# Performance work log

Measured on AMD Instinct MI355X. Metric: run time of the kernel, lower is better.

The kernel has to match this reference:

```python
import jax, jax.numpy as jnp
import numpy as np

SUB_NO = 20
T_NO = 200
T_DATA = 200000
E_NO = 400
I_NO = 100
N_BASIS = 20
COS_SHIFT = 1.0
COS_SCALE = 5.0


def make_cos_basis():
    # (N_BASIS, T_NO) raised-cosine basis in log time
    i = jnp.arange(N_BASIS, dtype=jnp.float32)[:, None]
    phi = (jnp.pi / 2.0) * i
    x = jnp.arange(T_NO, dtype=jnp.float32)[None, :]
    raw = COS_SCALE * jnp.log(x + COS_SHIFT)
    basis = 0.5 * jnp.cos(raw - phi) + 0.5
    keep = (raw >= phi - jnp.pi) & (raw <= phi + jnp.pi)
    return jnp.where(keep, basis, 0.0)


def grouped_causal_conv(syn, kern_flipped):
    # syn: (T, sub), kern_flipped: (sub, T_NO) already time-reversed -> causal filter
    x = jnp.pad(syn.T, ((0, 0), (T_NO - 1, 0)))[None]          # (1, sub, T+T_NO-1)
    out = jax.lax.conv_general_dilated(
        x, kern_flipped[:, None, :], (1,), 'VALID',
        dimension_numbers=('NCH', 'OIH', 'NCH'),
        feature_group_count=syn.shape[1])
    return out[0].T                                             # (T, sub)


def causal_conv1(z_pad, kern_flipped):
    # z_pad: (L,), kern_flipped: (T_NO,) -> valid conv, length L - T_NO + 1
    out = jax.lax.conv_general_dilated(
        z_pad[None, None, :], kern_flipped[None, None, :], (1,), 'VALID',
        dimension_numbers=('NCH', 'OIH', 'NCH'))
    return out[0, 0]


def setup_inputs() -> dict:
    key = jax.random.key(0)
    ks = jax.random.split(key, 12)
    S_e = (jax.random.uniform(ks[0], (T_DATA, E_NO)) < 0.05).astype(jnp.float32)
    S_i = (jax.random.uniform(ks[1], (T_DATA, I_NO)) < 0.05).astype(jnp.float32)
    Z = (jax.random.uniform(ks[2], (T_DATA,)) < 0.02).astype(jnp.float32)
    # binary-tree dendrite adjacency
    C_den = np.zeros((SUB_NO, SUB_NO), dtype=np.int32)
    for c in range(1, SUB_NO):
        C_den[(c - 1) // 2, c] = 1
    C_den = jnp.asarray(C_den)
    e_asn = np.asarray(jax.random.randint(ks[3], (E_NO,), 0, SUB_NO))
    i_asn = np.asarray(jax.random.randint(ks[4], (I_NO,), 0, SUB_NO))
    C_syn_e = np.zeros((SUB_NO, E_NO), dtype=np.float32); C_syn_e[e_asn, np.arange(E_NO)] = 1.0
    C_syn_i = np.zeros((SUB_NO, I_NO), dtype=np.float32); C_syn_i[i_asn, np.arange(I_NO)] = 1.0
    W_syn_ns = jax.random.uniform(ks[5], (SUB_NO, 2)) * 0.1
    W_syn_ns = W_syn_ns.at[:, 1].multiply(-1.0)
    return {
        'S_e': S_e, 'S_i': S_i, 'Z': Z,
        'C_den': C_den,
        'C_syn_e': jnp.asarray(C_syn_e), 'C_syn_i': jnp.asarray(C_syn_i),
        'W_syn_ns': W_syn_ns,
        'Tau_syn_ns': jnp.ones((SUB_NO, 2)) * 3.0,
        'Delta_syn_ns': jnp.zeros((SUB_NO, 2)),
        'W_syn_s': jax.random.normal(ks[6], (SUB_NO, N_BASIS, 2)) * 0.01,
        'W_sub_ns': jnp.ones(SUB_NO) * 0.1,
        'W_sub_s': jnp.ones(SUB_NO) * 0.1,
        'V_o': jax.random.normal(ks[7], (1,)),
        'Theta_ns': jnp.zeros(SUB_NO),
        'Theta_s': jnp.zeros(SUB_NO),
        'hist_s_weights': jax.random.normal(ks[8], (N_BASIS,)) * 0.01,
        'hist_ns_weights': jax.random.normal(ks[9], (N_BASIS,)) * 0.01,
    }


def reference(S_e, S_i, Z, C_den, C_syn_e, C_syn_i, W_syn_ns, Tau_syn_ns,
              Delta_syn_ns, W_syn_s, W_sub_ns, W_sub_s, V_o, Theta_ns,
              Theta_s, hist_s_weights, hist_ns_weights):
    cos_basis = make_cos_basis()
    # --- spike_convolve ---
    syn_e = S_e @ C_syn_e.T                                     # (T, sub)
    syn_i = S_i @ C_syn_i.T
    t = jnp.arange(T_NO, dtype=jnp.float32)[None, :]
    tau_e = Tau_syn_ns[:, 0:1] ** 2
    tau_i = Tau_syn_ns[:, 1:2] ** 2
    t_e = jnp.maximum(t - Delta_syn_ns[:, 0:1], 0.0) / tau_e
    t_i = jnp.maximum(t - Delta_syn_ns[:, 1:2], 0.0) / tau_i
    e_kern_ns = t_e * jnp.exp(-t_e) * W_syn_ns[:, 0:1] ** 2      # (sub, T_NO)
    i_kern_ns = -t_i * jnp.exp(-t_i) * W_syn_ns[:, 1:2] ** 2
    e_kern_s = (W_syn_s[:, :, 0] ** 2) @ cos_basis               # (sub, T_NO)
    i_kern_s = -(W_syn_s[:, :, 1] ** 2) @ cos_basis
    filt_e_ns = grouped_causal_conv(syn_e, jnp.flip(e_kern_ns, 1))
    filt_i_ns = grouped_causal_conv(syn_i, jnp.flip(i_kern_ns, 1))
    filt_e_s = grouped_causal_conv(syn_e, jnp.flip(e_kern_s, 1))
    filt_i_s = grouped_causal_conv(syn_i, jnp.flip(i_kern_s, 1))
    syn_ns = filt_e_ns + filt_i_ns
    syn_s = filt_e_s + filt_i_s
    # --- spike-history filtering of observed root spikes Z ---
    hist_s_kern = hist_s_weights @ cos_basis                     # (T_NO,)
    hist_ns_kern = hist_ns_weights @ cos_basis
    Z_pad = jnp.pad(Z, (T_NO, 0))                                # (T + T_NO,)
    hist_ns_filt = causal_conv1(Z_pad, jnp.flip(hist_ns_kern))[:-1]  # (T,)
    hist_s_filt = causal_conv1(Z_pad, jnp.flip(hist_s_kern))[:-1]
    # --- leaf-to-root tree recursion (unrolled over SUB_NO static nodes) ---
    C_den_f = C_den.astype(syn_s.dtype)
    w_s2 = W_sub_s ** 2
    w_ns2 = W_sub_ns ** 2
    T_data = S_e.shape[0]
    s_out = jnp.zeros((T_data, SUB_NO), dtype=syn_s.dtype)
    ns_out = jnp.zeros((T_data, SUB_NO), dtype=syn_ns.dtype)
    for idx in range(SUB_NO - 1, 0, -1):
        child_s = s_out @ (C_den_f[idx] * w_s2)                  # (T,) 0 if leaf
        child_ns = ns_out @ (C_den_f[idx] * w_ns2)
        s_out = s_out.at[:, idx].set(jnp.tanh(syn_s[:, idx] + child_s + Theta_s[idx]))
        ns_out = ns_out.at[:, idx].set(jnp.tanh(syn_ns[:, idx] + child_ns + Theta_ns[idx]))
    root_child_s = s_out @ (C_den_f[0] * w_s2)
    root_child_ns = ns_out @ (C_den_f[0] * w_ns2)
    s0 = jax.nn.sigmoid(hist_s_filt + syn_s[:, 0] + root_child_s + Theta_s[0])
    ns0 = jnp.tanh(hist_ns_filt + syn_ns[:, 0] + root_child_ns + Theta_ns[0])
    final_V = ns0 * w_ns2[0] + V_o
    final_Z = s0
    out_filters = jnp.vstack((e_kern_ns, i_kern_ns, e_kern_s, i_kern_s,
                              hist_ns_kern[None, :], hist_s_kern[None, :]))
    return final_V, final_Z, out_filters
```

## Files before the change

### kernel.cpp

```cpp
#include <hip/hip_runtime.h>

#define T_DATA 200000
#define E_NO 400
#define I_NO 100
#define SUB_NO 20
#define N_BASIS 20
#define T_NO 200

typedef unsigned short u16;
typedef unsigned int u32;

#define WS_K4    0
#define WS_HIST2 64000
#define WS_LISTS 65600
#define WS_SYNE  131072
#define WS_SYNI  (WS_SYNE + 8000000)
#define WS_SNS   (WS_SYNI + 8000000)
#define WS_SS    (WS_SNS + 8000000)
#define WS_NEED  (WS_SS + 8000000)

__device__ __forceinline__ u16 f2bf(float f) {
    union { float f; u32 u; } v; v.f = f;
    u32 u = v.u;
    u32 lsb = (u >> 16) & 1u;
    u += 0x7fffu + lsb;
    return (u16)(u >> 16);
}
__device__ __forceinline__ float bf2f(u16 b) {
    union { u32 u; float f; } v; v.u = ((u32)b) << 16; return v.f;
}
__device__ __forceinline__ void unpack8(uint4 u, float* x) {
    union { u32 u; float f; } c;
    c.u = u.x << 16;          x[0] = c.f;
    c.u = u.x & 0xffff0000u;  x[1] = c.f;
    c.u = u.y << 16;          x[2] = c.f;
    c.u = u.y & 0xffff0000u;  x[3] = c.f;
    c.u = u.z << 16;          x[4] = c.f;
    c.u = u.z & 0xffff0000u;  x[5] = c.f;
    c.u = u.w << 16;          x[6] = c.f;
    c.u = u.w & 0xffff0000u;  x[7] = c.f;
}
__device__ __forceinline__ float fast_tanh(float x) {
    x = fminf(fmaxf(x, -15.f), 15.f);
    float e = __expf(2.f * x);
    return 1.f - 2.f / (e + 1.f);
}
__device__ __forceinline__ float fast_sigmoid(float x) {
    x = fminf(fmaxf(x, -30.f), 30.f);
    return 1.f / (1.f + __expf(-x));
}

__global__ __launch_bounds__(256) void k_lists(
    const float* __restrict__ Cse, const float* __restrict__ Csi,
    int* __restrict__ lists)
{
    __shared__ int easn[E_NO], iasn[I_NO];
    __shared__ int cnt[2 * SUB_NO], cur[2 * SUB_NO];
    const int tid = threadIdx.x;
    if (tid < 2 * SUB_NO) cnt[tid] = 0;
    __syncthreads();
    for (int j = tid; j < E_NO; j += 256) {
        int a = 0;
        for (int s = 0; s < SUB_NO; ++s)
            if (Cse[s * E_NO + j] > 0.5f) a = s;
        easn[j] = a;
        atomicAdd(&cnt[a], 1);
    }
    for (int j = tid; j < I_NO; j += 256) {
        int a = 0;
        for (int s = 0; s < SUB_NO; ++s)
            if (Csi[s * I_NO + j] > 0.5f) a = s;
        iasn[j] = a;
        atomicAdd(&cnt[SUB_NO + a], 1);
    }
    __syncthreads();
    if (tid == 0) {
        int aE = 0, aI = 0;
        for (int s = 0; s < SUB_NO; ++s) {
            lists[s] = aE;      cur[s] = aE;           aE += cnt[s];
            lists[21 + s] = aI; cur[SUB_NO + s] = aI;  aI += cnt[SUB_NO + s];
        }
        lists[20] = aE;
        lists[41] = aI;
    }
    __syncthreads();
    for (int j = tid; j < E_NO; j += 256) {
        int p = atomicAdd(&cur[easn[j]], 1);
        lists[42 + p] = j;
    }
    for (int j = tid; j < I_NO; j += 256) {
        int p = atomicAdd(&cur[SUB_NO + iasn[j]], 1);
        lists[442 + p] = j;
    }
}

__global__ __launch_bounds__(256) void k_filters(
    const float* __restrict__ Wns, const float* __restrict__ Tau,
    const float* __restrict__ Del, const float* __restrict__ Wsyns,
    const float* __restrict__ HwS, const float* __restrict__ HwNS,
    float4* __restrict__ k4, float2* __restrict__ hist2,
    float* __restrict__ outF)
{
    __shared__ float cb[N_BASIS * T_NO];
    const int tid = threadIdx.x;
    const int b = blockIdx.x;
    const float PI = 3.14159265358979323846f;

    for (int it = tid; it < N_BASIS * T_NO; it += 256) {
        int bb = it / T_NO, j = it - bb * T_NO;
        float phi = 1.57079632679489662f * (float)bb;
        float raw = 5.0f * logf((float)j + 1.0f);
        float v = 0.f;
        if (raw >= phi - PI && raw <= phi + PI) v = 0.5f * cosf(raw - phi) + 0.5f;
        cb[it] = v;
    }
    __syncthreads();

    if (b < 20) {
        const int s = b;
        if (tid < T_NO) {
            const int j = tid;
            float tau_e = Tau[s * 2 + 0]; tau_e *= tau_e;
            float tau_i = Tau[s * 2 + 1]; tau_i *= tau_i;
            float de = Del[s * 2 + 0], di = Del[s * 2 + 1];
            float we = Wns[s * 2 + 0]; we *= we;
            float wi = Wns[s * 2 + 1]; wi *= wi;
            float te = fmaxf((float)j - de, 0.f) / tau_e;
            float ti = fmaxf((float)j - di, 0.f) / tau_i;
            float eNs = te * expf(-te) * we;
            float iNs = -ti * expf(-ti) * wi;
            float eS = 0.f, iS = 0.f;
            for (int bb = 0; bb < N_BASIS; ++bb) {
                float w0 = Wsyns[(s * N_BASIS + bb) * 2 + 0];
                float w1 = Wsyns[(s * N_BASIS + bb) * 2 + 1];
                float c = cb[bb * T_NO + j];
                eS += w0 * w0 * c;
                iS -= w1 * w1 * c;
            }
            int it = s * T_NO + j;
            k4[it] = make_float4(eNs, iNs, eS, iS);
            outF[it]         = eNs;
            outF[4000 + it]  = iNs;
            outF[8000 + it]  = eS;
            outF[12000 + it] = iS;
        }
    } else {
        if (tid < T_NO) {
            const int j = tid;
            float hn = 0.f, hs = 0.f;
            for (int bb = 0; bb < N_BASIS; ++bb) {
                float c = cb[bb * T_NO + j];
                hn += HwNS[bb] * c;
                hs += HwS[bb] * c;
            }
            hist2[j] = make_float2(hn, hs);
            outF[16000 + j] = hn;
            outF[16200 + j] = hs;
        }
    }
}

#define AR 16
__global__ __launch_bounds__(256) void k_spikes(
    const float* __restrict__ Se, const float* __restrict__ Si,
    const int* __restrict__ listsg,
    u16* __restrict__ synEb, u16* __restrict__ synIb)
{
    __shared__ __align__(16) float tE[AR * 404];
    __shared__ __align__(16) float tI[AR * 104];
    __shared__ int leo[21], lio[21];
    __shared__ u16 lei[E_NO], lii[I_NO];
    const int tid = threadIdx.x;
    const int t0 = blockIdx.x * AR;

    if (tid < 21) { leo[tid] = listsg[tid]; lio[tid] = listsg[21 + tid]; }
    for (int k = tid; k < E_NO; k += 256) lei[k] = (u16)listsg[42 + k];
    for (int k = tid; k < I_NO; k += 256) lii[k] = (u16)listsg[442 + k];

    const float4* Se4 = (const float4*)(Se + (size_t)t0 * E_NO);
    const float4* Si4 = (const float4*)(Si + (size_t)t0 * I_NO);
    for (int k = tid; k < AR * 100; k += 256) {
        int r = k / 100, c = k - r * 100;
        ((float4*)tE)[r * 101 + c] = Se4[k];
    }
    for (int k = tid; k < AR * 25; k += 256) {
        int r = k / 25, c = k - r * 25;
        ((float4*)tI)[r * 26 + c] = Si4[k];
    }
    __syncthreads();

    for (int task = tid; task < AR * SUB_NO; task += 256) {
        int s = task >> 4, r = task & 15;
        int k0 = leo[s], k1 = leo[s + 1];
        const float* row = tE + r * 404;
        float a0 = 0.f, a1 = 0.f, a2 = 0.f, a3 = 0.f;
        int k = k0;
        for (; k + 4 <= k1; k += 4) {
            a0 += row[lei[k]];
            a1 += row[lei[k + 1]];
            a2 += row[lei[k + 2]];
            a3 += row[lei[k + 3]];
        }
        for (; k < k1; ++k) a0 += row[lei[k]];
        synEb[(size_t)s * T_DATA + t0 + r] = f2bf((a0 + a1) + (a2 + a3));
    }
    for (int task = tid; task < AR * SUB_NO; task += 256) {
        int s = task >> 4, r = task & 15;
        const float* row = tI + r * 104;
        float a = 0.f;
        for (int k = lio[s]; k < lio[s + 1]; ++k) a += row[lii[k]];
        synIb[(size_t)s * T_DATA + t0 + r] = f2bf(a);
    }
}

#define TT 512
#define WROW 712
__global__ __launch_bounds__(256) void k_conv(
    const u16* __restrict__ synEb, const u16* __restrict__ synIb,
    const float4* __restrict__ k4g,
    u16* __restrict__ synNSb, u16* __restrict__ synSb)
{
    __shared__ __align__(16) u16 wE[4 * WROW];
    __shared__ __align__(16) u16 wI[4 * WROW];
    __shared__ __align__(16) float4 k4l[4 * T_NO];
    const int tid = threadIdx.x;
    const int t0 = blockIdx.x * TT;
    const int g  = blockIdx.y;
    const int W0 = t0 - 200;

    for (int q = tid; q < 712; q += 256) {
        int arr = (q >= 356) ? 1 : 0;
        int qq = q - arr * 356;
        int row = qq / 89, c = qq - row * 89;
        int s = g * 4 + row;
        const u16* src = (arr ? synIb : synEb) + (size_t)s * T_DATA;
        u16* dst = (arr ? wI : wE) + row * WROW + c * 8;
        int gg = W0 + c * 8;
        if (gg >= 0 && gg + 8 <= T_DATA) {
            *(uint4*)dst = *(const uint4*)(src + gg);
        } else {
            for (int e = 0; e < 8; ++e) {
                int t = gg + e;
                dst[e] = (t >= 0 && t < T_DATA) ? src[t] : (u16)0;
            }
        }
    }
    for (int q = tid; q < 800; q += 256) {
        int su = q / 200, j = q - su * 200;
        k4l[q] = k4g[(g * 4 + su) * T_NO + j];
    }
    __syncthreads();

    const int wv = tid >> 6;
    const int slot = tid & 63;
    const int bT = slot * 8;
    const int s = g * 4 + wv;
    const u16* rowE = wE + wv * WROW;
    const u16* rowI = wI + wv * WROW;

    float aN[8], aS2[8];
#pragma unroll
    for (int m = 0; m < 8; ++m) { aN[m] = 0.f; aS2[m] = 0.f; }

#pragma unroll 1
    for (int jj = 0; jj <= 192; jj += 8) {
        const int p = bT + 192 - jj;
        float xe[16], xi[16];
        uint4 eA = *(const uint4*)(rowE + p);
        uint4 eB = *(const uint4*)(rowE + p + 8);
        uint4 iA = *(const uint4*)(rowI + p);
        uint4 iB = *(const uint4*)(rowI + p + 8);
        unpack8(eA, xe); unpack8(eB, xe + 8);
        unpack8(iA, xi); unpack8(iB, xi + 8);
#pragma unroll
        for (int k = 0; k < 8; ++k) {
            float4 kk = k4l[wv * T_NO + jj + k];
#pragma unroll
            for (int m = 0; m < 8; ++m) {
                float e = xe[m + 8 - k];
                float ii = xi[m + 8 - k];
                aN[m]  = fmaf(e, kk.x, fmaf(ii, kk.y, aN[m]));
                aS2[m] = fmaf(e, kk.z, fmaf(ii, kk.w, aS2[m]));
            }
        }
    }

    const int t = t0 + bT;
    u32 w0 = (u32)f2bf(aN[0]) | ((u32)f2bf(aN[1]) << 16);
    u32 w1 = (u32)f2bf(aN[2]) | ((u32)f2bf(aN[3]) << 16);
    u32 w2 = (u32)f2bf(aN[4]) | ((u32)f2bf(aN[5]) << 16);
    u32 w3 = (u32)f2bf(aN[6]) | ((u32)f2bf(aN[7]) << 16);
    u32 v0 = (u32)f2bf(aS2[0]) | ((u32)f2bf(aS2[1]) << 16);
    u32 v1 = (u32)f2bf(aS2[2]) | ((u32)f2bf(aS2[3]) << 16);
    u32 v2 = (u32)f2bf(aS2[4]) | ((u32)f2bf(aS2[5]) << 16);
    u32 v3 = (u32)f2bf(aS2[6]) | ((u32)f2bf(aS2[7]) << 16);
    if (t + 8 <= T_DATA) {
        *(uint4*)(synNSb + (size_t)s * T_DATA + t) = make_uint4(w0, w1, w2, w3);
        *(uint4*)(synSb  + (size_t)s * T_DATA + t) = make_uint4(v0, v1, v2, v3);
    } else if (t < T_DATA) {
        u16 nv[8] = { f2bf(aN[0]), f2bf(aN[1]), f2bf(aN[2]), f2bf(aN[3]),
                      f2bf(aN[4]), f2bf(aN[5]), f2bf(aN[6]), f2bf(aN[7]) };
        u16 sv[8] = { f2bf(aS2[0]), f2bf(aS2[1]), f2bf(aS2[2]), f2bf(aS2[3]),
                      f2bf(aS2[4]), f2bf(aS2[5]), f2bf(aS2[6]), f2bf(aS2[7]) };
        for (int m = 0; m < 8 && t + m < T_DATA; ++m) {
            synNSb[(size_t)s * T_DATA + t + m] = nv[m];
            synSb[(size_t)s * T_DATA + t + m] = sv[m];
        }
    }
}

#define CT 256
__global__ __launch_bounds__(256) void k_tree(
    const u16* __restrict__ synNSb, const u16* __restrict__ synSb,
    const float* __restrict__ Z, const float2* __restrict__ hist2g,
    const int* __restrict__ Cden,
    const float* __restrict__ WsubNS, const float* __restrict__ WsubS,
    const float* __restrict__ Vo, const float* __restrict__ ThNS,
    const float* __restrict__ ThS,
    float* __restrict__ outV, float* __restrict__ outZ)
{
    __shared__ __align__(16) u16 lNS[SUB_NO * CT];
    __shared__ __align__(16) u16 lS[SUB_NO * CT];
    __shared__ float Zw[456];
    __shared__ float2 hl[T_NO];
    __shared__ float AS[SUB_NO][SUB_NO], AN[SUB_NO][SUB_NO];
    __shared__ float ths[SUB_NO], thn[SUB_NO];
    __shared__ float wn20s, vos;
    const int tid = threadIdx.x;
    const int t0 = blockIdx.x * CT;

    for (int q = tid; q < 1280; q += 256) {
        int arr = (q >= 640) ? 1 : 0;
        int qq = q - arr * 640;
        int row = qq >> 5, c = qq & 31;
        const u16* src = (arr ? synSb : synNSb) + (size_t)row * T_DATA;
        u16* dst = (arr ? lS : lNS) + row * CT + c * 8;
        int gg = t0 + c * 8;
        if (gg + 8 <= T_DATA) {
            *(uint4*)dst = *(const uint4*)(src + gg);
        } else {
            for (int e = 0; e < 8; ++e) {
                int t = gg + e;
                dst[e] = (t < T_DATA) ? src[t] : (u16)0;
            }
        }
    }
    for (int k = tid; k < 456; k += 256) {
        int t = t0 - 200 + k;
        Zw[k] = (t >= 0 && t < T_DATA) ? Z[t] : 0.f;
    }
    if (tid < T_NO) hl[tid] = hist2g[tid];
    for (int k = tid; k < SUB_NO * SUB_NO; k += 256) {
        int idx = k / SUB_NO, c = k - idx * SUB_NO;
        float m = (float)Cden[k];
        float wsv = WsubS[c];
        float wnv = WsubNS[c];
        AS[idx][c] = m * wsv * wsv;
        AN[idx][c] = m * wnv * wnv;
    }
    if (tid < SUB_NO) { ths[tid] = ThS[tid]; thn[tid] = ThNS[tid]; }
    if (tid == 0) {
        float w = WsubNS[0];
        wn20s = w * w;
        vos = Vo[0];
    }
    __syncthreads();

    const int t = t0 + tid;
    float hn = 0.f, hs = 0.f;
    for (int j = 0; j < T_NO; ++j) {
        float2 h = hl[j];
        float z = Zw[tid + 199 - j];
        hn = fmaf(h.x, z, hn);
        hs = fmaf(h.y, z, hs);
    }

    float vs[SUB_NO], vn[SUB_NO];
#pragma unroll
    for (int c = 0; c < SUB_NO; ++c) { vs[c] = 0.f; vn[c] = 0.f; }
#pragma unroll
    for (int idx = SUB_NO - 1; idx >= 1; --idx) {
        float cs = 0.f, cn = 0.f;
#pragma unroll
        for (int c = 0; c < SUB_NO; ++c) {
            cs = fmaf(AS[idx][c], vs[c], cs);
            cn = fmaf(AN[idx][c], vn[c], cn);
        }
        float synS_v = bf2f(lS[idx * CT + tid]);
        float synN_v = bf2f(lNS[idx * CT + tid]);
        vs[idx] = fast_tanh(synS_v + cs + ths[idx]);
        vn[idx] = fast_tanh(synN_v + cn + thn[idx]);
    }
    float cs0 = 0.f, cn0 = 0.f;
#pragma unroll
    for (int c = 0; c < SUB_NO; ++c) {
        cs0 = fmaf(AS[0][c], vs[c], cs0);
        cn0 = fmaf(AN[0][c], vn[c], cn0);
    }
    float s0  = fast_sigmoid(hs + bf2f(lS[tid]) + cs0 + ths[0]);
    float ns0 = fast_tanh(hn + bf2f(lNS[tid]) + cn0 + thn[0]);

    if (t < T_DATA) {
        outV[t] = ns0 * wn20s + vos;
        outZ[t] = s0;
    }
}

__global__ __launch_bounds__(256) void k_fused(
    const float* __restrict__ Se, const float* __restrict__ Si,
    const float* __restrict__ Z,
    const float4* __restrict__ k4g, const float2* __restrict__ hist2g,
    const int* __restrict__ listsg,
    const int* __restrict__ Cden,
    const float* __restrict__ WsubNS, const float* __restrict__ WsubS,
    const float* __restrict__ Vo, const float* __restrict__ ThNS,
    const float* __restrict__ ThS,
    float* __restrict__ outV, float* __restrict__ outZ)
{
    __shared__ __align__(16) u16 sE[SUB_NO * WROW];
    __shared__ __align__(16) u16 sI[SUB_NO * WROW];
    __shared__ __align__(16) float scr[4032];
    __shared__ float AS[SUB_NO][SUB_NO], AN[SUB_NO][SUB_NO];
    __shared__ float ths[SUB_NO], thn[SUB_NO];
    __shared__ int leo[21], lio[21];
    __shared__ u16 lei[E_NO], lii[I_NO];
    __shared__ float wn20s, vos;
    const int tid = threadIdx.x;
    const int t0 = blockIdx.x * TT;
    const int W0 = t0 - 200;

    if (tid < 21) { leo[tid] = listsg[tid]; lio[tid] = listsg[21 + tid]; }
    for (int k = tid; k < E_NO; k += 256) lei[k] = (u16)listsg[42 + k];
    for (int k = tid; k < I_NO; k += 256) lii[k] = (u16)listsg[442 + k];
    for (int k = tid; k < SUB_NO * SUB_NO; k += 256) {
        int idx = k / SUB_NO, c = k - idx * SUB_NO;
        float m = (float)Cden[k];
        float wsv = WsubS[c];
        float wnv = WsubNS[c];
        AS[idx][c] = m * wsv * wsv;
        AN[idx][c] = m * wnv * wnv;
    }
    if (tid < SUB_NO) { ths[tid] = ThS[tid]; thn[tid] = ThNS[tid]; }
    if (tid == 0) {
        float w = WsubNS[0];
        wn20s = w * w;
        vos = Vo[0];
    }

    const float4* Se4 = (const float4*)Se;
    const float4* Si4 = (const float4*)Si;
    float4* scr4 = (float4*)scr;
    float4 pre[4];

#define LOAD_TILE(IT)                                                        \
    {                                                                        \
        _Pragma("unroll")                                                    \
        for (int q = 0; q < 4; ++q) {                                        \
            int k = tid + q * 256;                                           \
            float4 v = make_float4(0.f, 0.f, 0.f, 0.f);                      \
            if (k < 800) {                                                   \
                int r = k / 100, c = k - r * 100;                            \
                int t = W0 + (IT) * 8 + r;                                   \
                if (t >= 0 && t < T_DATA) v = Se4[t * 100 + c];              \
            } else if (k < 1000) {                                           \
                int kk = k - 800;                                            \
                int r = kk / 25, c = kk - r * 25;                            \
                int t = W0 + (IT) * 8 + r;                                   \
                if (t >= 0 && t < T_DATA) v = Si4[t * 25 + c];               \
            }                                                                \
            pre[q] = v;                                                      \
        }                                                                    \
    }

#define STORE_TILE()                                                         \
    {                                                                        \
        _Pragma("unroll")                                                    \
        for (int q = 0; q < 4; ++q) {                                        \
            int k = tid + q * 256;                                           \
            if (k < 800) {                                                   \
                scr4[k] = pre[q];                                            \
            } else if (k < 1000) {                                           \
                int kk = k - 800;                                            \
                int r = kk / 25, c = kk - r * 25;                            \
                scr4[800 + r * 26 + c] = pre[q];                             \
            }                                                                \
        }                                                                    \
    }

#define GATHER(IT)                                                           \
    {                                                                        \
        for (int task = tid; task < 320; task += 256) {                      \
            if (task < 160) {                                                \
                int r = task / 20, s = task - r * 20;                        \
                int k0 = leo[s], k1 = leo[s + 1];                            \
                const int bb = r * 400;                                      \
                float a0 = 0.f, a1 = 0.f, a2 = 0.f, a3 = 0.f;                \
                int k = k0;                                                  \
                for (; k + 4 <= k1; k += 4) {                                \
                    a0 += scr[bb + lei[k]];                                  \
                    a1 += scr[bb + lei[k + 1]];                              \
                    a2 += scr[bb + lei[k + 2]];                              \
                    a3 += scr[bb + lei[k + 3]];                              \
                }                                                            \
                for (; k < k1; ++k) a0 += scr[bb + lei[k]];                  \
                sE[s * WROW + (IT) * 8 + r] = f2bf((a0 + a1) + (a2 + a3));   \
            } else {                                                         \
                int tk = task - 160;                                         \
                int r = tk / 20, s = tk - r * 20;                            \
                int k0 = lio[s], k1 = lio[s + 1];                            \
                const int bb = 3200 + r * 104;                               \
                float a0 = 0.f;                                              \
                for (int k = k0; k < k1; ++k) a0 += scr[bb + lii[k]];        \
                sI[s * WROW + (IT) * 8 + r] = f2bf(a0);                      \
            }                                                                \
        }                                                                    \
    }

    LOAD_TILE(0);
    STORE_TILE();
    __syncthreads();
#pragma unroll 1
    for (int it = 1; it < 89; ++it) {
        LOAD_TILE(it);
        GATHER(it - 1);
        __syncthreads();
        STORE_TILE();
        __syncthreads();
    }
    GATHER(88);
    __syncthreads();

    for (int k = tid; k < WROW; k += 256) {
        int t = W0 + k;
        scr[k] = (t >= 0 && t < T_DATA) ? Z[t] : 0.f;
    }
    {
        float2* hl = (float2*)(scr + WROW);
        for (int k = tid; k < T_NO; k += 256) hl[k] = hist2g[k];
    }
    __syncthreads();
    float hn0 = 0.f, hs0 = 0.f, hn1 = 0.f, hs1 = 0.f;
    {
        const float2* hl = (const float2*)(scr + WROW);
        const int i0 = tid * 2;
        for (int j = 0; j < T_NO; ++j) {
            float2 h = hl[j];
            float za = scr[i0 + 199 - j];
            float zb = scr[i0 + 200 - j];
            hn0 = fmaf(h.x, za, hn0); hs0 = fmaf(h.y, za, hs0);
            hn1 = fmaf(h.x, zb, hn1); hs1 = fmaf(h.y, zb, hs1);
        }
    }
    __syncthreads();

    const int wv = tid >> 6;
    const int slot = tid & 63;
    const int bT = slot * 8;
    float4* k4c = (float4*)scr;

#pragma unroll 1
    for (int g = 0; g < 5; ++g) {
        for (int q = tid; q < 800; q += 256) {
            int su = q / 200, j = q - su * 200;
            k4c[q] = k4g[(g * 4 + su) * T_NO + j];
        }
        __syncthreads();

        const int s = g * 4 + wv;
        const u16* rowE = sE + s * WROW;
        const u16* rowI = sI + s * WROW;
        float aN[8], aS2[8];
#pragma unroll
        for (int m = 0; m < 8; ++m) { aN[m] = 0.f; aS2[m] = 0.f; }

#pragma unroll 1
        for (int jj = 0; jj <= 192; jj += 8) {
            const int p = bT + 192 - jj;
            float xe[16], xi[16];
            uint4 eA = *(const uint4*)(rowE + p);
            uint4 eB = *(const uint4*)(rowE + p + 8);
            uint4 iA = *(const uint4*)(rowI + p);
            uint4 iB = *(const uint4*)(rowI + p + 8);
            unpack8(eA, xe); unpack8(eB, xe + 8);
            unpack8(iA, xi); unpack8(iB, xi + 8);
#pragma unroll
            for (int k = 0; k < 8; ++k) {
                float4 kk = k4c[wv * 200 + jj + k];
#pragma unroll
                for (int m = 0; m < 8; ++m) {
                    float e = xe[m + 8 - k];
                    float ii = xi[m + 8 - k];
                    aN[m]  = fmaf(e, kk.x, fmaf(ii, kk.y, aN[m]));
                    aS2[m] = fmaf(e, kk.z, fmaf(ii, kk.w, aS2[m]));
                }
            }
        }
        __syncthreads();
        {
            u32 w0 = (u32)f2bf(aN[0]) | ((u32)f2bf(aN[1]) << 16);
            u32 w1 = (u32)f2bf(aN[2]) | ((u32)f2bf(aN[3]) << 16);
            u32 w2 = (u32)f2bf(aN[4]) | ((u32)f2bf(aN[5]) << 16);
            u32 w3 = (u32)f2bf(aN[6]) | ((u32)f2bf(aN[7]) << 16);
            *(uint4*)(sE + s * WROW + bT) = make_uint4(w0, w1, w2, w3);
            u32 v0 = (u32)f2bf(aS2[0]) | ((u32)f2bf(aS2[1]) << 16);
            u32 v1 = (u32)f2bf(aS2[2]) | ((u32)f2bf(aS2[3]) << 16);
            u32 v2 = (u32)f2bf(aS2[4]) | ((u32)f2bf(aS2[5]) << 16);
            u32 v3 = (u32)f2bf(aS2[6]) | ((u32)f2bf(aS2[7]) << 16);
            *(uint4*)(sI + s * WROW + bT) = make_uint4(v0, v1, v2, v3);
        }
    }
    __syncthreads();

#pragma unroll 1
    for (int m = 0; m < 2; ++m) {
        const int i = tid * 2 + m;
        const int t = t0 + i;
        const float hfn = (m == 0) ? hn0 : hn1;
        const float hfs = (m == 0) ? hs0 : hs1;

        float vs[SUB_NO], vn[SUB_NO];
#pragma unroll
        for (int c = 0; c < SUB_NO; ++c) { vs[c] = 0.f; vn[c] = 0.f; }
#pragma unroll
        for (int idx = SUB_NO - 1; idx >= 1; --idx) {
            float cs = 0.f, cn = 0.f;
#pragma unroll
            for (int c = 0; c < SUB_NO; ++c) {
                cs = fmaf(AS[idx][c], vs[c], cs);
                cn = fmaf(AN[idx][c], vn[c], cn);
            }
            float synS_v = bf2f(sI[idx * WROW + i]);
            float synN_v = bf2f(sE[idx * WROW + i]);
            vs[idx] = fast_tanh(synS_v + cs + ths[idx]);
            vn[idx] = fast_tanh(synN_v + cn + thn[idx]);
        }
        float cs0 = 0.f, cn0 = 0.f;
#pragma unroll
        for (int c = 0; c < SUB_NO; ++c) {
            cs0 = fmaf(AS[0][c], vs[c], cs0);
            cn0 = fmaf(AN[0][c], vn[c], cn0);
        }
        float s0  = fast_sigmoid(hfs + bf2f(sI[i]) + cs0 + ths[0]);
        float ns0 = fast_tanh(hfn + bf2f(sE[i]) + cn0 + thn[0]);

        if (t < T_DATA) {
            outV[t] = ns0 * wn20s + vos;
            outZ[t] = s0;
        }
    }
}

extern "C" void kernel_launch(void* const* d_in, const int* in_sizes, int n_in,
                              void* d_out, int out_size, void* d_ws, size_t ws_size,
                              hipStream_t stream)
{
    const float* Se    = (const float*)d_in[0];
    const float* Si    = (const float*)d_in[1];
    const float* Z     = (const float*)d_in[2];
    const int*   Cden  = (const int*)d_in[3];
    const float* Cse   = (const float*)d_in[4];
    const float* Csi   = (const float*)d_in[5];
    const float* Wns   = (const float*)d_in[6];
    const float* Tau   = (const float*)d_in[7];
    const float* Del   = (const float*)d_in[8];
    const float* Wsyns = (const float*)d_in[9];
    const float* WsubNS= (const float*)d_in[10];
    const float* WsubS = (const float*)d_in[11];
    const float* Vo    = (const float*)d_in[12];
    const float* ThNS  = (const float*)d_in[13];
    const float* ThS   = (const float*)d_in[14];
    const float* HwS   = (const float*)d_in[15];
    const float* HwNS  = (const float*)d_in[16];

    char* ws = (char*)d_ws;
    float4* k4    = (float4*)(ws + WS_K4);
    float2* hist2 = (float2*)(ws + WS_HIST2);
    int*    lists = (int*)(ws + WS_LISTS);

    float* outV = (float*)d_out;
    float* outZ = outV + T_DATA;
    float* outF = outV + 2 * T_DATA;

    k_lists<<<1, 256, 0, stream>>>(Cse, Csi, lists);
    k_filters<<<21, 256, 0, stream>>>(Wns, Tau, Del, Wsyns, HwS, HwNS,
                                      k4, hist2, outF);

    if (ws_size >= (size_t)WS_NEED) {
        u16* synEb  = (u16*)(ws + WS_SYNE);
        u16* synIb  = (u16*)(ws + WS_SYNI);
        u16* synNSb = (u16*)(ws + WS_SNS);
        u16* synSb  = (u16*)(ws + WS_SS);
        k_spikes<<<T_DATA / AR, 256, 0, stream>>>(Se, Si, lists, synEb, synIb);
        dim3 gc((T_DATA + TT - 1) / TT, 5);
        k_conv<<<gc, 256, 0, stream>>>(synEb, synIb, k4, synNSb, synSb);
        k_tree<<<(T_DATA + CT - 1) / CT, 256, 0, stream>>>(
            synNSb, synSb, Z, hist2, Cden, WsubNS, WsubS, Vo, ThNS, ThS,
            outV, outZ);
    } else {
        k_fused<<<(T_DATA + TT - 1) / TT, 256, 0, stream>>>(
            Se, Si, Z, k4, hist2, lists, Cden, WsubNS, WsubS, Vo, ThNS, ThS,
            outV, outZ);
    }
}
```

Before: 659.6 us.

## Move history filter into conv kernel and merge setup kernels

Merges the list-building and filter-building kernels into one launch, with an extra block handling the synapse lists. Moves the 200-tap history convolution over Z out of the tree kernel into an extra grid row of the conv kernel, reusing its bf16 sliding-window FMA loop and writing the filtered history to a new workspace buffer. This removes a serial per-thread 200-step loop and its shared-memory staging from the tree kernel, and saves one launch. In exchange, Z and the history filter are rounded to bf16, three of the four waves in the extra block do wasted zero work, and extra global traffic is added for the new buffer.

```diff
diff --git a/kernel.cpp b/kernel.cpp
--- a/kernel.cpp
+++ b/kernel.cpp
@@ -17,7 +17,8 @@
 #define WS_SYNI  (WS_SYNE + 8000000)
 #define WS_SNS   (WS_SYNI + 8000000)
 #define WS_SS    (WS_SNS + 8000000)
-#define WS_NEED  (WS_SS + 8000000)
+#define WS_HF    (WS_SS + 8000000)
+#define WS_NEED  (WS_HF + 1600000)
 
 __device__ __forceinline__ u16 f2bf(float f) {
     union { float f; u32 u; } v; v.f = f;
@@ -50,61 +51,59 @@
     return 1.f / (1.f + __expf(-x));
 }
 
-__global__ __launch_bounds__(256) void k_lists(
+__global__ __launch_bounds__(256) void k_setup(
+    const float* __restrict__ Wns, const float* __restrict__ Tau,
+    const float* __restrict__ Del, const float* __restrict__ Wsyns,
+    const float* __restrict__ HwS, const float* __restrict__ HwNS,
     const float* __restrict__ Cse, const float* __restrict__ Csi,
-    int* __restrict__ lists)
+    float4* __restrict__ k4, float2* __restrict__ hist2,
+    int* __restrict__ lists, float* __restrict__ outF)
 {
+    __shared__ float cb[N_BASIS * T_NO];
     __shared__ int easn[E_NO], iasn[I_NO];
     __shared__ int cnt[2 * SUB_NO], cur[2 * SUB_NO];
     const int tid = threadIdx.x;
-    if (tid < 2 * SUB_NO) cnt[tid] = 0;
-    __syncthreads();
-    for (int j = tid; j < E_NO; j += 256) {
-        int a = 0;
-        for (int s = 0; s < SUB_NO; ++s)
-            if (Cse[s * E_NO + j] > 0.5f) a = s;
-        easn[j] = a;
-        atomicAdd(&cnt[a], 1);
-    }
-    for (int j = tid; j < I_NO; j += 256) {
-        int a = 0;
-        for (int s = 0; s < SUB_NO; ++s)
-            if (Csi[s * I_NO + j] > 0.5f) a = s;
-        iasn[j] = a;
-        atomicAdd(&cnt[SUB_NO + a], 1);
-    }
-    __syncthreads();
-    if (tid == 0) {
-        int aE = 0, aI = 0;
-        for (int s = 0; s < SUB_NO; ++s) {
-            lists[s] = aE;      cur[s] = aE;           aE += cnt[s];
-            lists[21 + s] = aI; cur[SUB_NO + s] = aI;  aI += cnt[SUB_NO + s];
-        }
-        lists[20] = aE;
-        lists[41] = aI;
-    }
-    __syncthreads();
-    for (int j = tid; j < E_NO; j += 256) {
-        int p = atomicAdd(&cur[easn[j]], 1);
-        lists[42 + p] = j;
-    }
-    for (int j = tid; j < I_NO; j += 256) {
-        int p = atomicAdd(&cur[SUB_NO + iasn[j]], 1);
-        lists[442 + p] = j;
-    }
-}
-
-__global__ __launch_bounds__(256) void k_filters(
-    const float* __restrict__ Wns, const float* __restrict__ Tau,
-    const float* __restrict__ Del, const float* __restrict__ Wsyns,
-    const float* __restrict__ HwS, const float* __restrict__ HwNS,
-    float4* __restrict__ k4, float2* __restrict__ hist2,
-    float* __restrict__ outF)
-{
-    __shared__ float cb[N_BASIS * T_NO];
-    const int tid = threadIdx.x;
     const int b = blockIdx.x;
     const float PI = 3.14159265358979323846f;
+
+    if (b == 21) {
+        if (tid < 2 * SUB_NO) cnt[tid] = 0;
+        __syncthreads();
+        for (int j = tid; j < E_NO; j += 256) {
+            int a = 0;
+            for (int s = 0; s < SUB_NO; ++s)
+                if (Cse[s * E_NO + j] > 0.5f) a = s;
+            easn[j] = a;
+            atomicAdd(&cnt[a], 1);
+        }
+        for (int j = tid; j < I_NO; j += 256) {
+            int a = 0;
+            for (int s = 0; s < SUB_NO; ++s)
+                if (Csi[s * I_NO + j] > 0.5f) a = s;
+            iasn[j] = a;
+            atomicAdd(&cnt[SUB_NO + a], 1);
+        }
+        __syncthreads();
+        if (tid == 0) {
+            int aE = 0, aI = 0;
+            for (int s = 0; s < SUB_NO; ++s) {
+                lists[s] = aE;      cur[s] = aE;           aE += cnt[s];
+                lists[21 + s] = aI; cur[SUB_NO + s] = aI;  aI += cnt[SUB_NO + s];
+            }
+            lists[20] = aE;
+            lists[41] = aI;
+        }
+        __syncthreads();
+        for (int j = tid; j < E_NO; j += 256) {
+            int p = atomicAdd(&cur[easn[j]], 1);
+            lists[42 + p] = j;
+        }
+        for (int j = tid; j < I_NO; j += 256) {
+            int p = atomicAdd(&cur[SUB_NO + iasn[j]], 1);
+            lists[442 + p] = j;
+        }
+        return;
+    }
 
     for (int it = tid; it < N_BASIS * T_NO; it += 256) {
         int bb = it / T_NO, j = it - bb * T_NO;
@@ -217,8 +216,10 @@
 #define WROW 712
 __global__ __launch_bounds__(256) void k_conv(
     const u16* __restrict__ synEb, const u16* __restrict__ synIb,
-    const float4* __restrict__ k4g,
-    u16* __restrict__ synNSb, u16* __restrict__ synSb)
+    const float* __restrict__ Z,
+    const float4* __restrict__ k4g, const float2* __restrict__ hist2g,
+    u16* __restrict__ synNSb, u16* __restrict__ synSb,
+    float2* __restrict__ hfilt)
 {
     __shared__ __align__(16) u16 wE[4 * WROW];
     __shared__ __align__(16) u16 wI[4 * WROW];
@@ -228,33 +229,61 @@
     const int g  = blockIdx.y;
     const int W0 = t0 - 200;
 
-    for (int q = tid; q < 712; q += 256) {
-        int arr = (q >= 356) ? 1 : 0;
-        int qq = q - arr * 356;
-        int row = qq / 89, c = qq - row * 89;
-        int s = g * 4 + row;
-        const u16* src = (arr ? synIb : synEb) + (size_t)s * T_DATA;
-        u16* dst = (arr ? wI : wE) + row * WROW + c * 8;
-        int gg = W0 + c * 8;
-        if (gg >= 0 && gg + 8 <= T_DATA) {
-            *(uint4*)dst = *(const uint4*)(src + gg);
-        } else {
+    if (g < 5) {
+        for (int q = tid; q < 712; q += 256) {
+            int arr = (q >= 356) ? 1 : 0;
+            int qq = q - arr * 356;
+            int row = qq / 89, c = qq - row * 89;
+            int s = g * 4 + row;
+            const u16* src = (arr ? synIb : synEb) + (size_t)s * T_DATA;
+            u16* dst = (arr ? wI : wE) + row * WROW + c * 8;
+            int gg = W0 + c * 8;
+            if (gg >= 0 && gg + 8 <= T_DATA) {
+                *(uint4*)dst = *(const uint4*)(src + gg);
+            } else {
+                for (int e = 0; e < 8; ++e) {
+                    int t = gg + e;
+                    dst[e] = (t >= 0 && t < T_DATA) ? src[t] : (u16)0;
+                }
+            }
+        }
+        for (int q = tid; q < 800; q += 256) {
+            int su = q / 200, j = q - su * 200;
+            k4l[q] = k4g[(g * 4 + su) * T_NO + j];
+        }
+    } else {
+        for (int q = tid; q < 623; q += 256) {
+            if (q < 356) ((uint4*)wI)[q] = make_uint4(0, 0, 0, 0);
+            else         ((uint4*)wE)[q - 356 + 89] = make_uint4(0, 0, 0, 0);
+        }
+        for (int c = tid; c < 89; c += 256) {
+            int gg = W0 + c * 8;
+            u16 zb[8];
             for (int e = 0; e < 8; ++e) {
                 int t = gg + e;
-                dst[e] = (t >= 0 && t < T_DATA) ? src[t] : (u16)0;
-            }
-        }
-    }
-    for (int q = tid; q < 800; q += 256) {
-        int su = q / 200, j = q - su * 200;
-        k4l[q] = k4g[(g * 4 + su) * T_NO + j];
+                zb[e] = (t >= 0 && t < T_DATA) ? f2bf(Z[t]) : (u16)0;
+            }
+            u32 w0 = (u32)zb[0] | ((u32)zb[1] << 16);
+            u32 w1 = (u32)zb[2] | ((u32)zb[3] << 16);
+            u32 w2 = (u32)zb[4] | ((u32)zb[5] << 16);
+            u32 w3 = (u32)zb[6] | ((u32)zb[7] << 16);
+            *(uint4*)(wE + c * 8) = make_uint4(w0, w1, w2, w3);
+        }
+        for (int q = tid; q < 800; q += 256) {
+            int su = q / 200, j = q - su * 200;
+            float4 v = make_float4(0.f, 0.f, 0.f, 0.f);
+            if (su == 0) {
+                float2 h = hist2g[j];
+                v = make_float4(h.x, 0.f, h.y, 0.f);
+            }
+            k4l[q] = v;
+        }
     }
     __syncthreads();
 
     const int wv = tid >> 6;
     const int slot = tid & 63;
     const int bT = slot * 8;
-    const int s = g * 4 + wv;
     const u16* rowE = wE + wv * WROW;
     const u16* rowI = wI + wv * WROW;
 
@@ -285,34 +314,40 @@
         }
     }
 
-    const int t = t0 + bT;
-    u32 w0 = (u32)f2bf(aN[0]) | ((u32)f2bf(aN[1]) << 16);
-    u32 w1 = (u32)f2bf(aN[2]) | ((u32)f2bf(aN[3]) << 16);
-    u32 w2 = (u32)f2bf(aN[4]) | ((u32)f2bf(aN[5]) << 16);
-    u32 w3 = (u32)f2bf(aN[6]) | ((u32)f2bf(aN[7]) << 16);
-    u32 v0 = (u32)f2bf(aS2[0]) | ((u32)f2bf(aS2[1]) << 16);
-    u32 v1 = (u32)f2bf(aS2[2]) | ((u32)f2bf(aS2[3]) << 16);
-    u32 v2 = (u32)f2bf(aS2[4]) | ((u32)f2bf(aS2[5]) << 16);
-    u32 v3 = (u32)f2bf(aS2[6]) | ((u32)f2bf(aS2[7]) << 16);
-    if (t + 8 <= T_DATA) {
-        *(uint4*)(synNSb + (size_t)s * T_DATA + t) = make_uint4(w0, w1, w2, w3);
-        *(uint4*)(synSb  + (size_t)s * T_DATA + t) = make_uint4(v0, v1, v2, v3);
-    } else if (t < T_DATA) {
-        u16 nv[8] = { f2bf(aN[0]), f2bf(aN[1]), f2bf(aN[2]), f2bf(aN[3]),
-                      f2bf(aN[4]), f2bf(aN[5]), f2bf(aN[6]), f2bf(aN[7]) };
-        u16 sv[8] = { f2bf(aS2[0]), f2bf(aS2[1]), f2bf(aS2[2]), f2bf(aS2[3]),
-                      f2bf(aS2[4]), f2bf(aS2[5]), f2bf(aS2[6]), f2bf(aS2[7]) };
-        for (int m = 0; m < 8 && t + m < T_DATA; ++m) {
-            synNSb[(size_t)s * T_DATA + t + m] = nv[m];
-            synSb[(size_t)s * T_DATA + t + m] = sv[m];
-        }
+    if (g < 5) {
+        const int s = g * 4 + wv;
+        const int t = t0 + bT;
+        u32 w0 = (u32)f2bf(aN[0]) | ((u32)f2bf(aN[1]) << 16);
+        u32 w1 = (u32)f2bf(aN[2]) | ((u32)f2bf(aN[3]) << 16);
+        u32 w2 = (u32)f2bf(aN[4]) | ((u32)f2bf(aN[5]) << 16);
+        u32 w3 = (u32)f2bf(aN[6]) | ((u32)f2bf(aN[7]) << 16);
+        u32 v0 = (u32)f2bf(aS2[0]) | ((u32)f2bf(aS2[1]) << 16);
+        u32 v1 = (u32)f2bf(aS2[2]) | ((u32)f2bf(aS2[3]) << 16);
+        u32 v2 = (u32)f2bf(aS2[4]) | ((u32)f2bf(aS2[5]) << 16);
+        u32 v3 = (u32)f2bf(aS2[6]) | ((u32)f2bf(aS2[7]) << 16);
+        if (t + 8 <= T_DATA) {
+            *(uint4*)(synNSb + (size_t)s * T_DATA + t) = make_uint4(w0, w1, w2, w3);
+            *(uint4*)(synSb  + (size_t)s * T_DATA + t) = make_uint4(v0, v1, v2, v3);
+        } else if (t < T_DATA) {
+            for (int m = 0; m < 8 && t + m < T_DATA; ++m) {
+                synNSb[(size_t)s * T_DATA + t + m] = f2bf(aN[m]);
+                synSb[(size_t)s * T_DATA + t + m] = f2bf(aS2[m]);
+            }
+        }
+    } else if (wv == 0) {
+#pragma unroll
+        for (int m = 0; m < 8; ++m) {
+            int tt = t0 + bT + m + 1;
+            if (tt < T_DATA) hfilt[tt] = make_float2(aN[m], aS2[m]);
+        }
+        if (blockIdx.x == 0 && tid == 0) hfilt[0] = make_float2(0.f, 0.f);
     }
 }
 
 #define CT 256
 __global__ __launch_bounds__(256) void k_tree(
     const u16* __restrict__ synNSb, const u16* __restrict__ synSb,
-    const float* __restrict__ Z, const float2* __restrict__ hist2g,
+    const float2* __restrict__ hfilt,
     const int* __restrict__ Cden,
     const float* __restrict__ WsubNS, const float* __restrict__ WsubS,
     const float* __restrict__ Vo, const float* __restrict__ ThNS,
@@ -321,8 +356,6 @@
 {
     __shared__ __align__(16) u16 lNS[SUB_NO * CT];
     __shared__ __align__(16) u16 lS[SUB_NO * CT];
-    __shared__ float Zw[456];
-    __shared__ float2 hl[T_NO];
     __shared__ float AS[SUB_NO][SUB_NO], AN[SUB_NO][SUB_NO];
     __shared__ float ths[SUB_NO], thn[SUB_NO];
     __shared__ float wn20s, vos;
@@ -345,11 +378,6 @@
             }
         }
     }
-    for (int k = tid; k < 456; k += 256) {
-        int t = t0 - 200 + k;
-        Zw[k] = (t >= 0 && t < T_DATA) ? Z[t] : 0.f;
-    }
-    if (tid < T_NO) hl[tid] = hist2g[tid];
     for (int k = tid; k < SUB_NO * SUB_NO; k += 256) {
         int idx = k / SUB_NO, c = k - idx * SUB_NO;
         float m = (float)Cden[k];
@@ -367,13 +395,8 @@
     __syncthreads();
 
     const int t = t0 + tid;
-    float hn = 0.f, hs = 0.f;
-    for (int j = 0; j < T_NO; ++j) {
-        float2 h = hl[j];
-        float z = Zw[tid + 199 - j];
-        hn = fmaf(h.x, z, hn);
-        hs = fmaf(h.y, z, hs);
-    }
+    float2 hf = make_float2(0.f, 0.f);
+    if (t < T_DATA) hf = hfilt[t];
 
     float vs[SUB_NO], vn[SUB_NO];
 #pragma unroll
@@ -397,8 +420,8 @@
         cs0 = fmaf(AS[0][c], vs[c], cs0);
         cn0 = fmaf(AN[0][c], vn[c], cn0);
     }
-    float s0  = fast_sigmoid(hs + bf2f(lS[tid]) + cs0 + ths[0]);
-    float ns0 = fast_tanh(hn + bf2f(lNS[tid]) + cn0 + thn[0]);
+    float s0  = fast_sigmoid(hf.y + bf2f(lS[tid]) + cs0 + ths[0]);
+    float ns0 = fast_tanh(hf.x + bf2f(lNS[tid]) + cn0 + thn[0]);
 
     if (t < T_DATA) {
         outV[t] = ns0 * wn20s + vos;
@@ -681,20 +704,21 @@
     float* outZ = outV + T_DATA;
     float* outF = outV + 2 * T_DATA;
 
-    k_lists<<<1, 256, 0, stream>>>(Cse, Csi, lists);
-    k_filters<<<21, 256, 0, stream>>>(Wns, Tau, Del, Wsyns, HwS, HwNS,
-                                      k4, hist2, outF);
+    k_setup<<<22, 256, 0, stream>>>(Wns, Tau, Del, Wsyns, HwS, HwNS, Cse, Csi,
+                                    k4, hist2, lists, outF);
 
     if (ws_size >= (size_t)WS_NEED) {
         u16* synEb  = (u16*)(ws + WS_SYNE);
         u16* synIb  = (u16*)(ws + WS_SYNI);
         u16* synNSb = (u16*)(ws + WS_SNS);
         u16* synSb  = (u16*)(ws + WS_SS);
+        float2* hfilt = (float2*)(ws + WS_HF);
         k_spikes<<<T_DATA / AR, 256, 0, stream>>>(Se, Si, lists, synEb, synIb);
-        dim3 gc((T_DATA + TT - 1) / TT, 5);
-        k_conv<<<gc, 256, 0, stream>>>(synEb, synIb, k4, synNSb, synSb);
+        dim3 gc((T_DATA + TT - 1) / TT, 6);
+        k_conv<<<gc, 256, 0, stream>>>(synEb, synIb, Z, k4, hist2,
+                                       synNSb, synSb, hfilt);
         k_tree<<<(T_DATA + CT - 1) / CT, 256, 0, stream>>>(
-            synNSb, synSb, Z, hist2, Cden, WsubNS, WsubS, Vo, ThNS, ThS,
+            synNSb, synSb, hfilt, Cden, WsubNS, WsubS, Vo, ThNS, ThS,
             outV, outZ);
     } else {
         k_fused<<<(T_DATA + TT - 1) / TT, 256, 0, stream>>>(
```

New measurement: 665.9 us. No clear change (+1.0%).
